# Optimization experiments

Hardware: AMD Instinct MI355X
Metric: run time of the kernel (lower is better)

The kernel has to match this reference:

```python
import jax, jax.numpy as jnp
import numpy as np

B, S, D = 2, 2048, 2048
H, HKV = 32, 8
DH = D // H          # 64
G = H // HKV         # group size 4


def setup_inputs() -> dict:
    key = jax.random.key(0)
    ks = jax.random.split(key, 5)
    sc = lambda fan_in: 1.0 / np.sqrt(fan_in)
    return {
        "hidden_states": jax.random.normal(ks[0], (B, S, D), jnp.float32),
        "Wq": jax.random.normal(ks[1], (D, D), jnp.float32) * sc(D),
        "bq": jnp.zeros((D,), jnp.float32),
        "Wk": jax.random.normal(ks[2], (D, HKV * DH), jnp.float32) * sc(D),
        "bk": jnp.zeros((HKV * DH,), jnp.float32),
        "Wv": jax.random.normal(ks[3], (D, HKV * DH), jnp.float32) * sc(D),
        "bv": jnp.zeros((HKV * DH,), jnp.float32),
        "Wo": jax.random.normal(ks[4], (D, D), jnp.float32) * sc(D),
        "bo": jnp.zeros((D,), jnp.float32),
    }


def reference(hidden_states, Wq, bq, Wk, bk, Wv, bv, Wo, bo):
    x = hidden_states
    # projections
    q = x @ Wq + bq                     # [B,S,D]
    k = x @ Wk + bk                     # [B,S,HKV*DH]
    v = x @ Wv + bv
    # split heads; group queries so K/V broadcast instead of repeat_interleave
    # (same math: repeat_interleave expands kv head j to query heads j*G..j*G+G-1)
    q = q.reshape(B, S, HKV, G, DH).transpose(0, 2, 3, 1, 4)  # [B,HKV,G,S,DH]
    k = k.reshape(B, S, HKV, DH).transpose(0, 2, 1, 3)        # [B,HKV,S,DH]
    v = v.reshape(B, S, HKV, DH).transpose(0, 2, 1, 3)
    scale = 1.0 / jnp.sqrt(jnp.asarray(DH, q.dtype))
    scores = jnp.einsum('bhgqd,bhkd->bhgqk', q, k) * scale    # [B,HKV,G,S,S]
    attn = jax.nn.softmax(scores, axis=-1)
    ctx = jnp.einsum('bhgqk,bhkd->bhgqd', attn, v)            # [B,HKV,G,S,DH]
    # merge heads back to [B,S,D] (head order = kv_head*G + group idx)
    merged = ctx.transpose(0, 3, 1, 2, 4).reshape(B, S, D)
    out = merged @ Wo + bo
    return out
```

## Files before the change

kernel.cpp:

```cpp
#include <hip/hip_runtime.h>
#include <cstdint>

typedef __bf16 bf16;
typedef __attribute__((ext_vector_type(8))) __bf16 bf16x8;
typedef __attribute__((ext_vector_type(4))) __bf16 bf16x4;
typedef __attribute__((ext_vector_type(2))) __bf16 bf16x2;
typedef __attribute__((ext_vector_type(4))) float f32x4;
typedef __attribute__((ext_vector_type(16))) float f32x16;

#define B_   2
#define S_   2048
#define D_   2048
#define HKV_ 8
#define H_   32
#define DH_  64

__device__ __forceinline__ void async_cp16(const bf16* g, bf16* l) {
  __builtin_amdgcn_global_load_lds(
      (__attribute__((address_space(1))) void*)g,
      (__attribute__((address_space(3))) void*)l,
      16, 0, 0);
}

__device__ __forceinline__ float fexp2(float x) {
#if __has_builtin(__builtin_amdgcn_exp2f)
  return __builtin_amdgcn_exp2f(x);
#else
  return __expf(x * 0.69314718056f);
#endif
}

__global__ __launch_bounds__(256) void transpose_k(
    const float* __restrict__ in, bf16* __restrict__ out, int R, int C) {
  __shared__ bf16 tile[64][65];
  const int tx = threadIdx.x & 63;
  const int ty = threadIdx.x >> 6;
  const int r0 = blockIdx.x * 64;
  const int c0 = blockIdx.y * 64;
#pragma unroll
  for (int j = 0; j < 16; ++j) {
    int r = j * 4 + ty;
    tile[r][tx] = (bf16)in[(size_t)(r0 + r) * C + c0 + tx];
  }
  __syncthreads();
#pragma unroll
  for (int j = 0; j < 16; ++j) {
    int r = j * 4 + ty;
    out[(size_t)(c0 + r) * R + r0 + tx] = tile[tx][r];
  }
}

template <typename AT, int OMODE>
__global__ __launch_bounds__(256) void gemm_bt(
    const AT* __restrict__ A, const bf16* __restrict__ Bt,
    const float* __restrict__ b1, const float* __restrict__ b2,
    const float* __restrict__ b3,
    void* __restrict__ C0, void* __restrict__ C1, void* __restrict__ C2,
    int N, int K) {
  __shared__ bf16 a_tile[128 * 64];
  __shared__ bf16 b_tile[128 * 64];
  const int tid  = threadIdx.x;
  const int wave = tid >> 6;
  const int lane = tid & 63;
  const int quad = lane >> 4;
  const int l16  = lane & 15;
  const int m0   = blockIdx.x * 128;
  const int n0   = blockIdx.y * 128;
  const int wm   = (wave >> 1) * 64;
  const int wn   = (wave & 1) * 64;

  f32x4 acc[4][4] = {};

  const int srow  = wave * 32 + (lane >> 3);
  const int skoff = (lane & 7) * 8;
  const AT*   Ag = A  + (size_t)(m0 + srow) * K + skoff;
  const bf16* Bg = Bt + (size_t)(n0 + srow) * K + skoff;
  bf16* al = &a_tile[srow * 64 + skoff];
  bf16* bl = &b_tile[srow * 64 + skoff];

  for (int kt = 0; kt < K; kt += 64) {
    bf16x8 areg[4];
    if constexpr (sizeof(AT) == 4) {
#pragma unroll
      for (int c = 0; c < 4; ++c) {
        const float* ap = (const float*)(Ag + (size_t)(c * 8) * K + kt);
        float4 lo = *(const float4*)ap;
        float4 hi = *(const float4*)(ap + 4);
        areg[c][0] = (bf16)lo.x; areg[c][1] = (bf16)lo.y;
        areg[c][2] = (bf16)lo.z; areg[c][3] = (bf16)lo.w;
        areg[c][4] = (bf16)hi.x; areg[c][5] = (bf16)hi.y;
        areg[c][6] = (bf16)hi.z; areg[c][7] = (bf16)hi.w;
      }
    }
    __syncthreads();
    if constexpr (sizeof(AT) == 4) {
#pragma unroll
      for (int c = 0; c < 4; ++c) *(bf16x8*)(al + c * 512) = areg[c];
    } else {
#pragma unroll
      for (int c = 0; c < 4; ++c)
        async_cp16((const bf16*)Ag + (size_t)(c * 8) * K + kt, al + c * 512);
    }
#pragma unroll
    for (int c = 0; c < 4; ++c)
      async_cp16(Bg + (size_t)(c * 8) * K + kt, bl + c * 512);
    __syncthreads();
#pragma unroll
    for (int kk = 0; kk < 64; kk += 32) {
      bf16x8 af[4], bfr[4];
#pragma unroll
      for (int i = 0; i < 4; ++i) {
        af[i]  = *(const bf16x8*)&a_tile[(wm + i * 16 + l16) * 64 + kk + quad * 8];
        bfr[i] = *(const bf16x8*)&b_tile[(wn + i * 16 + l16) * 64 + kk + quad * 8];
      }
#pragma unroll
      for (int i = 0; i < 4; ++i)
#pragma unroll
        for (int j = 0; j < 4; ++j)
          acc[i][j] = __builtin_amdgcn_mfma_f32_16x16x32_bf16(af[i], bfr[j], acc[i][j], 0, 0, 0);
    }
  }

#pragma unroll
  for (int i = 0; i < 4; ++i) {
    const int row = m0 + wm + i * 16 + quad * 4;
#pragma unroll
    for (int j = 0; j < 4; ++j) {
      const int col = n0 + wn + j * 16 + l16;
      if constexpr (OMODE == 2) {
        const float bia = b1[col];
#pragma unroll
        for (int r = 0; r < 4; ++r)
          ((float*)C0)[(size_t)(row + r) * N + col] = acc[i][j][r] + bia;
      } else {
        if (col < 2048) {
          const float bia = b1[col];
#pragma unroll
          for (int r = 0; r < 4; ++r)
            ((bf16*)C0)[(size_t)(row + r) * 2048 + col] =
                (bf16)((acc[i][j][r] + bia) * 0.18033688f);
        } else if (col < 2560) {
          const int cc = col - 2048;
          const float bia = b2[cc];
#pragma unroll
          for (int r = 0; r < 4; ++r)
            ((bf16*)C1)[(size_t)(row + r) * 512 + cc] = (bf16)(acc[i][j][r] + bia);
        } else {
          const int cc = col - 2560;
          const float bia = b3[cc];
          const int hh = cc >> 6, dd = cc & 63;
#pragma unroll
          for (int r = 0; r < 4; ++r) {
            const int rr = row + r;
            const int bb = rr >> 11, ss = rr & 2047;
            ((bf16*)C2)[((((size_t)bb * HKV_ + hh) * DH_ + dd) << 11) + ss] =
                (bf16)(acc[i][j][r] + bia);
          }
        }
      }
    }
  }
}

__global__ __launch_bounds__(256, 2) void gqa_flash(
    const bf16* __restrict__ Qs,
    const bf16* __restrict__ Kb,
    const bf16* __restrict__ VT,
    bf16* __restrict__ ctx) {
  __shared__ bf16 k_tile[2][128 * 64];
  __shared__ bf16 vt_tile[2][64 * 128];

  const int tid  = threadIdx.x;
  const int wave = tid >> 6;
  const int lane = tid & 63;
  const int l32  = lane & 31;
  const int hi   = lane >> 5;

  const int qt = blockIdx.x;
  const int hq = blockIdx.y;
  const int b  = blockIdx.z;
  const int h  = hq >> 2;

  const int r2 = (l32 & 7) ^ ((l32 >> 3) & 3);

  bf16x8 qf0[4], qf1[4];
  const int qrow0 = b * S_ + qt * 256 + wave * 64;
  {
    const bf16* qp = Qs + (size_t)(qrow0 + l32) * D_ + hq * DH_ + hi * 8;
#pragma unroll
    for (int ks = 0; ks < 4; ++ks) {
      qf0[ks] = *(const bf16x8*)(qp + ks * 16);
      qf1[ks] = *(const bf16x8*)(qp + (size_t)32 * D_ + ks * 16);
    }
  }

  f32x16 o0[2] = {}, o1[2] = {};
  float l_run0 = 0.f, l_run1 = 0.f;

  const int cg0 = (lane & 7) ^ ((lane >> 3) & 7);
  const int l4  = lane >> 4;
  const bf16* Kg0 = Kb + (size_t)(b * S_ + wave * 32 + (lane >> 3)) * (HKV_ * DH_) + h * DH_;
  const bf16* Vg0 = VT + ((size_t)(b * HKV_ + h) * DH_ + wave * 16 + l4) * S_;
  const int ldsl = wave * 2048 + lane * 8;

  auto stage = [&](int buf, int kt0) {
    bf16* kd = &k_tile[0][0] + buf * 8192 + ldsl;
    bf16* vd = &vt_tile[0][0] + buf * 8192 + ldsl;
#pragma unroll
    for (int c = 0; c < 4; ++c)
      async_cp16(Kg0 + (size_t)(kt0 + c * 8) * (HKV_ * DH_) + ((cg0 ^ c) << 3),
                 kd + c * 512);
#pragma unroll
    for (int c = 0; c < 4; ++c) {
      const int u   = c * 4 + l4;
      const int swz = (u & 7) ^ ((wave * 2 + (u >> 3)) & 3);
      const int cgv = (lane & 15) ^ swz;
      async_cp16(Vg0 + (size_t)(c * 4) * S_ + kt0 + (cgv << 3), vd + c * 512);
    }
  };

  stage(0, 0);
  __syncthreads();

  for (int t = 0; t < S_ / 128; ++t) {
    {
      const int tn = (t + 1) & (S_ / 128 - 1);
      stage((t + 1) & 1, tn * 128);
    }
    const bf16* ktile = k_tile[t & 1];
    const bf16* vtile = vt_tile[t & 1];

#pragma unroll
    for (int kb = 0; kb < 4; ++kb) {
      f32x16 st0 = {}, st1 = {};
#pragma unroll
      for (int ks = 0; ks < 4; ++ks) {
        bf16x8 kf = *(const bf16x8*)&ktile[(kb * 32 + l32) * 64 +
                                           (((ks * 2 + hi) ^ r2) << 3)];
        st0 = __builtin_amdgcn_mfma_f32_32x32x16_bf16(kf, qf0[ks], st0, 0, 0, 0);
        st1 = __builtin_amdgcn_mfma_f32_32x32x16_bf16(kf, qf1[ks], st1, 0, 0, 0);
      }

#pragma unroll
      for (int kqlo = 0; kqlo < 2; ++kqlo) {
        int wa[4], wb[4];
        float sm0 = 0.f, sm1 = 0.f;
#pragma unroll
        for (int e2 = 0; e2 < 4; ++e2) {
          const int e = 4 * kqlo + e2;
          const float a0 = fexp2(st0[2 * e]);
          const float a1 = fexp2(st0[2 * e + 1]);
          sm0 += a0 + a1;
          bf16x2 t0; t0[0] = (bf16)a0; t0[1] = (bf16)a1;
          wa[e2] = __builtin_bit_cast(int, t0);
          const float c0 = fexp2(st1[2 * e]);
          const float c1 = fexp2(st1[2 * e + 1]);
          sm1 += c0 + c1;
          bf16x2 t1; t1[0] = (bf16)c0; t1[1] = (bf16)c1;
          wb[e2] = __builtin_bit_cast(int, t1);
        }
        l_run0 += sm0;
        l_run1 += sm1;

        auto ra0 = __builtin_amdgcn_permlane32_swap(wa[0], wa[2], false, false);
        auto ra1 = __builtin_amdgcn_permlane32_swap(wa[1], wa[3], false, false);
        auto rb0 = __builtin_amdgcn_permlane32_swap(wb[0], wb[2], false, false);
        auto rb1 = __builtin_amdgcn_permlane32_swap(wb[1], wb[3], false, false);
        union { int wi[4]; bf16x8 v; } pb0, pb1;
        pb0.wi[0] = ra0[0]; pb0.wi[1] = ra1[0]; pb0.wi[2] = ra0[1]; pb0.wi[3] = ra1[1];
        pb1.wi[0] = rb0[0]; pb1.wi[1] = rb1[0]; pb1.wi[2] = rb0[1]; pb1.wi[3] = rb1[1];
        const int kq = kb * 2 + kqlo;
        const int gv = ((kq * 2 + hi) ^ r2) << 3;
#pragma unroll
        for (int jm = 0; jm < 2; ++jm) {
          bf16x8 av = *(const bf16x8*)&vtile[(jm * 32 + l32) * 128 + gv];
          o0[jm] = __builtin_amdgcn_mfma_f32_32x32x16_bf16(av, pb0.v, o0[jm], 0, 0, 0);
          o1[jm] = __builtin_amdgcn_mfma_f32_32x32x16_bf16(av, pb1.v, o1[jm], 0, 0, 0);
        }
      }
    }
    __syncthreads();
  }

  l_run0 += __shfl_xor(l_run0, 32);
  l_run1 += __shfl_xor(l_run1, 32);
  const float inv0 = 1.f / l_run0;
  const float inv1 = 1.f / l_run1;

  const size_t qrowA = (size_t)(qrow0 + l32);
  const size_t qrowB = qrowA + 32;
#pragma unroll
  for (int jm = 0; jm < 2; ++jm)
#pragma unroll
    for (int c = 0; c < 4; ++c) {
      bf16x4 ov;
#pragma unroll
      for (int j = 0; j < 4; ++j) ov[j] = (bf16)(o0[jm][4 * c + j] * inv0);
      const int dh0 = jm * 32 + c * 8 + hi * 4;
      *(bf16x4*)&ctx[qrowA * D_ + hq * DH_ + dh0] = ov;
#pragma unroll
      for (int j = 0; j < 4; ++j) ov[j] = (bf16)(o1[jm][4 * c + j] * inv1);
      *(bf16x4*)&ctx[qrowB * D_ + hq * DH_ + dh0] = ov;
    }
}

extern "C" void kernel_launch(void* const* d_in, const int* in_sizes, int n_in,
                              void* d_out, int out_size, void* d_ws, size_t ws_size,
                              hipStream_t stream) {
  const float* x  = (const float*)d_in[0];
  const float* Wq = (const float*)d_in[1];
  const float* bq = (const float*)d_in[2];
  const float* Wk = (const float*)d_in[3];
  const float* bk = (const float*)d_in[4];
  const float* Wv = (const float*)d_in[5];
  const float* bv = (const float*)d_in[6];
  const float* Wo = (const float*)d_in[7];
  const float* bo = (const float*)d_in[8];
  float* out = (float*)d_out;

  char* ws = (char*)d_ws;
  bf16* WT  = (bf16*)(ws);
  bf16* ctx = (bf16*)(ws);
  bf16* WoT = (bf16*)(ws + 16777216);
  bf16* Qs  = (bf16*)(ws + 25165824);
  bf16* Kb  = (bf16*)(ws + 41943040);
  bf16* VT  = (bf16*)(ws + 46137344);

  dim3 blk(256);
  transpose_k<<<dim3(32, 32), blk, 0, stream>>>(Wq, WT, 2048, 2048);
  transpose_k<<<dim3(32, 8),  blk, 0, stream>>>(Wk, WT + (size_t)2048 * 2048, 2048, 512);
  transpose_k<<<dim3(32, 8),  blk, 0, stream>>>(Wv, WT + (size_t)2560 * 2048, 2048, 512);
  transpose_k<<<dim3(32, 32), blk, 0, stream>>>(Wo, WoT, 2048, 2048);

  gemm_bt<float, 3><<<dim3(32, 24), blk, 0, stream>>>(
      x, WT, bq, bk, bv, Qs, Kb, VT, 3072, 2048);

  gqa_flash<<<dim3(8, 32, 2), blk, 0, stream>>>(Qs, Kb, VT, ctx);

  gemm_bt<bf16, 2><<<dim3(32, 16), blk, 0, stream>>>(
      ctx, WoT, bo, nullptr, nullptr, out, nullptr, nullptr, 2048, 2048);
}
```

Measured before the change: 339.3 us.

## Load V fragments directly from global memory, drop V LDS tile, raise occupancy

Removes the shared-memory staging of the transposed V tile and instead has each lane load its V MFMA operand straight from global memory (L2-cached) inside the inner loop. Halving LDS use allows launch bounds to be raised to 3 blocks per SM. It also wraps the MFMA groups in s_setprio to favour matrix issue over other waves. The cost is unhidden global-load latency on the critical path of the PV MFMAs, plus more VMEM traffic since the four waves each reload the same V data.

```diff
diff --git a/kernel.cpp b/kernel.cpp
--- a/kernel.cpp
+++ b/kernel.cpp
@@ -162,13 +162,12 @@
   }
 }
 
-__global__ __launch_bounds__(256, 2) void gqa_flash(
+__global__ __launch_bounds__(256, 3) void gqa_flash(
     const bf16* __restrict__ Qs,
     const bf16* __restrict__ Kb,
     const bf16* __restrict__ VT,
     bf16* __restrict__ ctx) {
   __shared__ bf16 k_tile[2][128 * 64];
-  __shared__ bf16 vt_tile[2][64 * 128];
 
   const int tid  = threadIdx.x;
   const int wave = tid >> 6;
@@ -198,41 +197,30 @@
   float l_run0 = 0.f, l_run1 = 0.f;
 
   const int cg0 = (lane & 7) ^ ((lane >> 3) & 7);
-  const int l4  = lane >> 4;
   const bf16* Kg0 = Kb + (size_t)(b * S_ + wave * 32 + (lane >> 3)) * (HKV_ * DH_) + h * DH_;
-  const bf16* Vg0 = VT + ((size_t)(b * HKV_ + h) * DH_ + wave * 16 + l4) * S_;
   const int ldsl = wave * 2048 + lane * 8;
+
+  const bf16* Vrow = VT + ((size_t)(b * HKV_ + h) * DH_ + l32) * S_ + hi * 8;
 
   auto stage = [&](int buf, int kt0) {
     bf16* kd = &k_tile[0][0] + buf * 8192 + ldsl;
-    bf16* vd = &vt_tile[0][0] + buf * 8192 + ldsl;
 #pragma unroll
     for (int c = 0; c < 4; ++c)
       async_cp16(Kg0 + (size_t)(kt0 + c * 8) * (HKV_ * DH_) + ((cg0 ^ c) << 3),
                  kd + c * 512);
-#pragma unroll
-    for (int c = 0; c < 4; ++c) {
-      const int u   = c * 4 + l4;
-      const int swz = (u & 7) ^ ((wave * 2 + (u >> 3)) & 3);
-      const int cgv = (lane & 15) ^ swz;
-      async_cp16(Vg0 + (size_t)(c * 4) * S_ + kt0 + (cgv << 3), vd + c * 512);
-    }
   };
 
   stage(0, 0);
   __syncthreads();
 
-  for (int t = 0; t < S_ / 128; ++t) {
-    {
-      const int tn = (t + 1) & (S_ / 128 - 1);
-      stage((t + 1) & 1, tn * 128);
-    }
-    const bf16* ktile = k_tile[t & 1];
-    const bf16* vtile = vt_tile[t & 1];
+  for (int kt = 0; kt < S_; kt += 128) {
+    stage(((kt >> 7) + 1) & 1, (kt + 128) & (S_ - 1));
+    const bf16* ktile = k_tile[(kt >> 7) & 1];
 
 #pragma unroll
     for (int kb = 0; kb < 4; ++kb) {
       f32x16 st0 = {}, st1 = {};
+      __builtin_amdgcn_s_setprio(1);
 #pragma unroll
       for (int ks = 0; ks < 4; ++ks) {
         bf16x8 kf = *(const bf16x8*)&ktile[(kb * 32 + l32) * 64 +
@@ -240,6 +228,7 @@
         st0 = __builtin_amdgcn_mfma_f32_32x32x16_bf16(kf, qf0[ks], st0, 0, 0, 0);
         st1 = __builtin_amdgcn_mfma_f32_32x32x16_bf16(kf, qf1[ks], st1, 0, 0, 0);
       }
+      __builtin_amdgcn_s_setprio(0);
 
 #pragma unroll
       for (int kqlo = 0; kqlo < 2; ++kqlo) {
@@ -269,14 +258,16 @@
         union { int wi[4]; bf16x8 v; } pb0, pb1;
         pb0.wi[0] = ra0[0]; pb0.wi[1] = ra1[0]; pb0.wi[2] = ra0[1]; pb0.wi[3] = ra1[1];
         pb1.wi[0] = rb0[0]; pb1.wi[1] = rb1[0]; pb1.wi[2] = rb0[1]; pb1.wi[3] = rb1[1];
-        const int kq = kb * 2 + kqlo;
-        const int gv = ((kq * 2 + hi) ^ r2) << 3;
-#pragma unroll
-        for (int jm = 0; jm < 2; ++jm) {
-          bf16x8 av = *(const bf16x8*)&vtile[(jm * 32 + l32) * 128 + gv];
-          o0[jm] = __builtin_amdgcn_mfma_f32_32x32x16_bf16(av, pb0.v, o0[jm], 0, 0, 0);
-          o1[jm] = __builtin_amdgcn_mfma_f32_32x32x16_bf16(av, pb1.v, o1[jm], 0, 0, 0);
-        }
+
+        const int koff = kt + kb * 32 + kqlo * 16;
+        bf16x8 av0 = *(const bf16x8*)(Vrow + koff);
+        bf16x8 av1 = *(const bf16x8*)(Vrow + (size_t)32 * S_ + koff);
+        __builtin_amdgcn_s_setprio(1);
+        o0[0] = __builtin_amdgcn_mfma_f32_32x32x16_bf16(av0, pb0.v, o0[0], 0, 0, 0);
+        o1[0] = __builtin_amdgcn_mfma_f32_32x32x16_bf16(av0, pb1.v, o1[0], 0, 0, 0);
+        o0[1] = __builtin_amdgcn_mfma_f32_32x32x16_bf16(av1, pb0.v, o0[1], 0, 0, 0);
+        o1[1] = __builtin_amdgcn_mfma_f32_32x32x16_bf16(av1, pb1.v, o1[1], 0, 0, 0);
+        __builtin_amdgcn_s_setprio(0);
       }
     }
     __syncthreads();
```

After: 529.2 us. +56.0%, slower.
